# Optimization experiments

Measured on AMD Instinct MI355X. Metric: run time of the kernel, lower is better.

## Reference

```python
import jax, jax.numpy as jnp
import numpy as np
from jax import lax

GAMMA = 1.0
T = 1.0
NEG = -1e30  # acts as -inf for logsumexp padding without producing NaNs in grads


def _dp_forward(D):
    """Soft-max (logsumexp) 2D DP: R[i,j] = D[i,j] + LSE(R[i-1,j-1], R[i-1,j], R[i,j-1]).
    D: [B, N, M] -> R: [B, N, M]. Implemented with a padded virtual row/col where
    R_pad[0,0]=0 and all other boundary cells are NEG (-inf surrogate)."""
    B, N, M = D.shape
    neg = jnp.full((B,), NEG, D.dtype)

    def row_step(prev, d_row):
        # prev: [B, M+1] padded previous row R_pad[i-1, :]; d_row: [B, M]
        diag = prev[:, :-1]  # R_pad[i-1, j]   (diagonal neighbor of cell j)
        up = prev[:, 1:]     # R_pad[i-1, j+1] (vertical neighbor)

        def col_step(left, xs):
            dg, u, d = xs  # each [B]; left = R_pad[i, j] (horizontal neighbor)
            m = jnp.maximum(jnp.maximum(dg, u), left)
            val = d + m + jnp.log(jnp.exp(dg - m) + jnp.exp(u - m) + jnp.exp(left - m))
            return val, val

        _, row = lax.scan(col_step, neg, (diag.T, up.T, d_row.T))  # row: [M, B]
        row = row.T  # [B, M]
        new_prev = jnp.concatenate([neg[:, None], row], axis=1)  # [B, M+1]
        return new_prev, row

    prev0 = jnp.concatenate(
        [jnp.zeros((B, 1), D.dtype), jnp.full((B, M), NEG, D.dtype)], axis=1
    )  # virtual row: R_pad[0,0]=0, rest -inf
    _, R = lax.scan(row_step, prev0, jnp.swapaxes(D, 0, 1))  # R: [N, B, M]
    return jnp.swapaxes(R, 0, 1)  # [B, N, M]


def setup_inputs() -> dict:
    key = jax.random.key(0)
    d = jax.random.normal(key, (64, 512, 512), dtype=jnp.float32)
    return {"d": d}


def reference(d):
    ds = d / GAMMA
    f = _dp_forward(ds)                           # forward-direction DP
    b = _dp_forward(ds[:, ::-1, ::-1])[:, ::-1, ::-1]  # reverse-direction DP, re-flipped
    logit = f + b - ds
    return GAMMA * (logit - logit.max()) / T
```

## Files before the change

### kernel.cpp

```cpp
#include <hip/hip_runtime.h>
#include <stdint.h>

#define NEGV -1e30f
static constexpr int BATCH = 64;
static constexpr int NN = 512;
static constexpr int MM = 512;
static constexpr int NM = NN * MM;
static constexpr size_t TOTAL = (size_t)BATCH * NM;
static constexpr int ROTC = 11;

typedef float f32x4 __attribute__((ext_vector_type(4)));

__device__ __forceinline__ int prow(int b, int k) {
    return (k + ROTC * b) & 511;
}

__device__ __forceinline__ float wave_shr1(float x) {
    int y = __builtin_amdgcn_mov_dpp(__float_as_int(x), 0x138, 0xf, 0xf, true);
    return __int_as_float(y);
}

#define F4C(v, c) ((c) == 0 ? (v).x : (c) == 1 ? (v).y : (c) == 2 ? (v).z : (v).w)

__device__ __forceinline__ int swz(int row, int c) {
    return row * 64 + ((((c >> 2) ^ (row & 15)) << 2) | (c & 3));
}

__device__ inline float blockMax256(float v) {
    __shared__ float sm[256];
    sm[threadIdx.x] = v;
    __syncthreads();
    for (int s = 128; s > 0; s >>= 1) {
        if ((int)threadIdx.x < s)
            sm[threadIdx.x] = fmaxf(sm[threadIdx.x], sm[threadIdx.x + s]);
        __syncthreads();
    }
    return sm[0];
}


__global__ __launch_bounds__(256) void skew_kernel(const float* __restrict__ D,
                                                   float* __restrict__ Sd) {
    __shared__ float lds[64 * 64];
    const int bi = blockIdx.x;
    const int b = bi >> 6;
    const int t = bi & 63;
    const int r0 = (t >> 3) * 64;
    const int c0 = (t & 7) * 64;
    const float* Db = D + (size_t)b * NM;
    float* So = Sd + (size_t)b * NM;
    {
        const int xg = (threadIdx.x & 15) * 4;
        const int y0 = threadIdx.x >> 4;
        for (int sw = 0; sw < 4; ++sw) {
            const int y = y0 + 16 * sw;
            const float4 v = *(const float4*)(Db + (size_t)(r0 + y) * MM + c0 + xg);
            *(float4*)(lds + swz(y, xg)) = v;
        }
    }
    __syncthreads();
    const int rp = (int)threadIdx.x & 63;
    const int s0 = (int)threadIdx.x >> 6;
    for (int it = 0; it < 32; ++it) {
        const int s = s0 + 4 * it;
        if (s >= 127) break;
        const int dcol = s - rp;
        if (dcol >= 0 && dcol < 64) {
            So[(size_t)prow(b, r0 + c0 + s) * MM + r0 + rp] = lds[swz(rp, dcol)];
        }
    }
}

#define LSE3(dg, up, lf, dd, out) do { \
    const float m_ = fmaxf(fmaxf((dg), (up)), (lf)); \
    const float mn_ = fminf(fminf((dg), (up)), (lf)); \
    const float md_ = __builtin_amdgcn_fmed3f((dg), (up), (lf)); \
    const float s_ = 1.f + __expf(mn_ - m_) + __expf(md_ - m_); \
    (out) = (dd) + m_ + __logf(s_); \
} while (0)

#define D0(RV) (DIR ? (RV)[3] : (RV)[0])
#define D1(RV) (DIR ? (RV)[2] : (RV)[1])
#define D2(RV) (DIR ? (RV)[1] : (RV)[2])
#define D3(RV) (DIR ? (RV)[0] : (RV)[3])

template <int DIR, int HALF>
__device__ __forceinline__ void dp_half(const float* __restrict__ Sdp,
                                        const int b, const int lane,
                                        float* __restrict__ ring,
                                        float2* __restrict__ pring,
                                        volatile int* my_prog,
                                        volatile int* other_prog,
                                        volatile int* w_prog) {
    constexpr int R0 = HALF * 256;
    const int t4 = lane * 4;
    const bool l0 = (lane == 0);

    float pA0 = NEGV, pA1 = NEGV, pA2 = NEGV, pA3 = NEGV;
    float pB0 = NEGV, pB1 = NEGV, pB2 = NEGV, pB3 = NEGV;
    f32x4 r0, r1, r2, r3, r4, r5, r6, r7;

#define RLOAD(kk, RV) do { \
        const int lr_ = DIR ? (510 - (kk)) : (kk); \
        const float* rp_ = Sdp + (size_t)prow(b, lr_) * MM; \
        const float* pa_ = DIR ? (rp_ + 508 - R0 - t4) : (rp_ + R0 + t4); \
        asm volatile("global_load_dwordx4 %0, %1, off" : "=v"(RV) : "v"(pa_)); \
    } while (0)

#define GATE() do { \
        asm volatile("s_waitcnt vmcnt(7)" ::: "memory"); \
        __builtin_amdgcn_sched_barrier(0); \
    } while (0)

#define STEP(PH, PA, PB, RV) do { \
        const int k = kb + (PH); \
        GATE(); \
        const float ups_ = wave_shr1(PA##3); \
        const float dgs_ = wave_shr1(PB##3); \
        float up0_, dg0_; \
        if constexpr (HALF == 0) { \
            up0_ = l0 ? NEGV : ups_; \
            dg0_ = l0 ? ((k == 0) ? 0.f : NEGV) : dgs_; \
        } else { \
            up0_ = l0 ? pr##PH.x : ups_; \
            dg0_ = l0 ? pr##PH.y : dgs_; \
        } \
        const float g1_ = PB##0, g2_ = PB##1, g3_ = PB##2; \
        LSE3(dg0_, up0_, PA##0, D0(RV), PB##0); \
        LSE3(g1_, PA##0, PA##1, D1(RV), PB##1); \
        LSE3(g2_, PA##1, PA##2, D2(RV), PB##2); \
        LSE3(g3_, PA##2, PA##3, D3(RV), PB##3); \
        *(float4*)(ring + ((k & 31) << 9) + R0 + t4) = \
            make_float4(PB##0, PB##1, PB##2, PB##3); \
        if constexpr (HALF == 0) { \
            if (lane == 63) pring[k & 31] = make_float2(PB##3, PA##3); \
        } \
        RLOAD(k + 8, RV); \
    } while (0)

    RLOAD(0, r0); RLOAD(1, r1); RLOAD(2, r2); RLOAD(3, r3);
    RLOAD(4, r4); RLOAD(5, r5); RLOAD(6, r6); RLOAD(7, r7);

    for (int kb = 0; kb < NN + MM; kb += 8) {
        if constexpr (HALF == 0) {
            while (*w_prog < kb - 24 || *other_prog < kb - 24)
                __builtin_amdgcn_s_sleep(2);
        } else {
            while (*other_prog < kb + 6 || *w_prog < kb - 24)
                __builtin_amdgcn_s_sleep(2);
        }
        asm volatile("" ::: "memory");
        float2 pr0 = make_float2(NEGV, NEGV), pr1 = pr0, pr2 = pr0, pr3 = pr0,
               pr4 = pr0, pr5 = pr0, pr6 = pr0, pr7 = pr0;
        if constexpr (HALF == 1) {
            pr0 = pring[(kb - 1) & 31]; pr1 = pring[(kb + 0) & 31];
            pr2 = pring[(kb + 1) & 31]; pr3 = pring[(kb + 2) & 31];
            pr4 = pring[(kb + 3) & 31]; pr5 = pring[(kb + 4) & 31];
            pr6 = pring[(kb + 5) & 31]; pr7 = pring[(kb + 6) & 31];
        }
        STEP(0, pA, pB, r0);
        STEP(1, pB, pA, r1);
        STEP(2, pA, pB, r2);
        STEP(3, pB, pA, r3);
        STEP(4, pA, pB, r4);
        STEP(5, pB, pA, r5);
        STEP(6, pA, pB, r6);
        STEP(7, pB, pA, r7);
        asm volatile("s_waitcnt lgkmcnt(0)" ::: "memory");
        if (l0) *my_prog = kb + 7;
    }

#undef STEP
#undef GATE
#undef RLOAD
}

__device__ __forceinline__ void writer_run(float* __restrict__ Sout, const int b,
                                           const int lane,
                                           const float* __restrict__ ring,
                                           volatile int* a_prog,
                                           volatile int* b_prog,
                                           volatile int* w_prog) {
    const int t8 = lane * 8;
    const int lg0 = lane * 8;
    const int lg1 = lane * 8 + 4;

    float4 v0_0, v1_0, v0_1, v1_1, v0_2, v1_2, v0_3, v1_3,
           v0_4, v1_4, v0_5, v1_5, v0_6, v1_6, v0_7, v1_7;

#define WROW(kk, V0, V1) do { \
        const int k_ = (kk); \
        const float* lp_ = ring + ((k_ & 31) << 9); \
        V0 = *(const float4*)(lp_ + lg0); \
        V1 = *(const float4*)(lp_ + lg1); \
        const int kt_ = k_ - t8; \
        float* sp_ = Sout + (size_t)prow(b, k_) * MM + t8; \
        if (kt_ >= 3 && kt_ <= 511) { \
            *(float4*)sp_ = V0; \
        } else if (kt_ >= 0 && kt_ <= 514) { \
            if (kt_ <= 511)             sp_[0] = V0.x; \
            if (kt_ >= 1 && kt_ <= 512) sp_[1] = V0.y; \
            if (kt_ >= 2 && kt_ <= 513) sp_[2] = V0.z; \
            if (kt_ >= 3)               sp_[3] = V0.w; \
        } \
        if (kt_ >= 7 && kt_ <= 515) { \
            *(float4*)(sp_ + 4) = V1; \
        } else if (kt_ >= 4 && kt_ <= 518) { \
            if (kt_ <= 515)             sp_[4] = V1.x; \
            if (kt_ >= 5 && kt_ <= 516) sp_[5] = V1.y; \
            if (kt_ >= 6 && kt_ <= 517) sp_[6] = V1.z; \
            if (kt_ >= 7)               sp_[7] = V1.w; \
        } \
    } while (0)

    for (int k0 = 0; k0 < NN + MM; k0 += 8) {
        while (*a_prog < k0 + 7 || *b_prog < k0 + 7) __builtin_amdgcn_s_sleep(2);
        asm volatile("" ::: "memory");
        WROW(k0 + 0, v0_0, v1_0);
        WROW(k0 + 1, v0_1, v1_1);
        WROW(k0 + 2, v0_2, v1_2);
        WROW(k0 + 3, v0_3, v1_3);
        WROW(k0 + 4, v0_4, v1_4);
        WROW(k0 + 5, v0_5, v1_5);
        WROW(k0 + 6, v0_6, v1_6);
        WROW(k0 + 7, v0_7, v1_7);
        asm volatile("s_waitcnt lgkmcnt(0)" ::: "memory");
        if (lane == 0) *w_prog = k0 + 7;
    }
#undef WROW
}

__global__ __launch_bounds__(192, 1) void dp_skew_kernel(const float* __restrict__ Sd,
                                                         float* __restrict__ Sf,
                                                         float* __restrict__ Sb) {
    __shared__ float ring[32 * 512];
    __shared__ float2 pring[32];
    __shared__ int ctrl[3];
    if (threadIdx.x == 0) { ctrl[0] = -1; ctrl[1] = -1; ctrl[2] = -1; }
    if (threadIdx.x < 32) pring[threadIdx.x] = make_float2(NEGV, NEGV);
    __syncthreads();

    volatile int* a_prog = &ctrl[0];
    volatile int* b_prog = &ctrl[1];
    volatile int* w_prog = &ctrl[2];

    const int blk = blockIdx.x;
    const int b = blk & (BATCH - 1);
    const int dir = blk >> 6;
    const int wid = (int)threadIdx.x >> 6;
    const int lane = (int)threadIdx.x & 63;
    const float* Sdb = Sd + (size_t)b * NM;
    float* Sout = (dir ? Sb : Sf) + (size_t)b * NM;

    if (wid == 0) {
        if (dir) dp_half<1, 0>(Sdb, b, lane, ring, pring, a_prog, b_prog, w_prog);
        else     dp_half<0, 0>(Sdb, b, lane, ring, pring, a_prog, b_prog, w_prog);
    } else if (wid == 1) {
        if (dir) dp_half<1, 1>(Sdb, b, lane, ring, pring, b_prog, a_prog, w_prog);
        else     dp_half<0, 1>(Sdb, b, lane, ring, pring, b_prog, a_prog, w_prog);
    } else {
        writer_run(Sout, b, lane, ring, a_prog, b_prog, w_prog);
    }
}

__global__ __launch_bounds__(256) void logit_skew_kernel(float* __restrict__ Sd,
                                                         const float* __restrict__ Sf,
                                                         const float* __restrict__ Sb,
                                                         float* __restrict__ partial) {
    const size_t n4 = TOTAL / 4;
    float mx = NEGV;
    const size_t stride = (size_t)gridDim.x * blockDim.x;
    for (size_t e = (size_t)blockIdx.x * blockDim.x + threadIdx.x; e < n4; e += stride) {
        const int b = (int)(e >> 16);
        const int rem = (int)(e & 65535);
        const int kp = rem >> 7;
        const int r4 = (rem & 127) << 2;
        const size_t base = (size_t)b * NM;
        const size_t idx = base + (size_t)prow(b, kp) * MM + r4;
        const float4 f = *(const float4*)(Sf + idx);
        const float4 d = *(const float4*)(Sd + idx);
        const int k2 = (510 - kp) & 511;
        const float4 bb = *(const float4*)(Sb + base + (size_t)prow(b, k2) * MM + (508 - r4));
        float4 v;
        v.x = f.x + bb.w - d.x;
        v.y = f.y + bb.z - d.y;
        v.z = f.z + bb.y - d.z;
        v.w = f.w + bb.x - d.w;
        *(float4*)(Sd + idx) = v;
        mx = fmaxf(mx, fmaxf(fmaxf(v.x, v.y), fmaxf(v.z, v.w)));
    }
    float bm = blockMax256(mx);
    if (threadIdx.x == 0) partial[blockIdx.x] = bm;
}

__global__ __launch_bounds__(256) void finalmax_kernel(const float* __restrict__ partial,
                                                       int n,
                                                       float* __restrict__ outmax) {
    float mx = NEGV;
    for (int i = threadIdx.x; i < n; i += 256) mx = fmaxf(mx, partial[i]);
    float bm = blockMax256(mx);
    if (threadIdx.x == 0) *outmax = bm;
}

__global__ __launch_bounds__(256) void unskew_kernel(const float* __restrict__ OS,
                                                     float* __restrict__ out,
                                                     const float* __restrict__ maxp) {
    __shared__ float lds[127 * 64];
    const float mx = *maxp;
    const int bi = blockIdx.x;
    const int b = bi >> 6;
    const int t = bi & 63;
    const int i0 = (t >> 3) * 64;
    const int j0 = (t & 7) * 64;
    const float* Ob = OS + (size_t)b * NM;
    float* ob = out + (size_t)b * NM;
    const int base = i0 + j0;
    {
        const int xg = ((int)threadIdx.x & 15) * 4;
        const int s0 = (int)threadIdx.x >> 4;
        for (int sw = 0; sw < 8; ++sw) {
            const int s = s0 + 16 * sw;
            if (s < 127) {
                const float4 v = *(const float4*)(Ob + (size_t)prow(b, base + s) * MM + i0 + xg);
                *(float4*)(lds + swz(s, xg)) = v;
            }
        }
    }
    __syncthreads();
    const int x4 = ((int)threadIdx.x & 15) * 4;
    const int y0 = (int)threadIdx.x >> 4;
    for (int sw = 0; sw < 4; ++sw) {
        const int y = y0 + 16 * sw;
        float4 v;
        v.x = lds[swz(x4 + 0 + y, y)] - mx;
        v.y = lds[swz(x4 + 1 + y, y)] - mx;
        v.z = lds[swz(x4 + 2 + y, y)] - mx;
        v.w = lds[swz(x4 + 3 + y, y)] - mx;
        *(float4*)(ob + (size_t)(i0 + y) * MM + j0 + x4) = v;
    }
}

template <int DIR>
__device__ __forceinline__ void dp_run_legacy(const float* __restrict__ Db,
                                              float* __restrict__ Rp, int lane) {
    const int i0 = lane * 8;
    const bool l0 = (lane == 0);
    const float dgb0 = l0 ? 0.f : NEGV;

#define PTRS(r) \
    const float* ldp_##r = DIR ? (Db + (size_t)(NM - 1) - (size_t)(i0 + r) * MM) \
                               : (Db + (size_t)(i0 + r) * MM); \
    float* stp_##r = DIR ? (Rp + (size_t)(NM - 1) - (size_t)(i0 + r) * MM) \
                         : (Rp + (size_t)(i0 + r) * MM);
    PTRS(0) PTRS(1) PTRS(2) PTRS(3) PTRS(4) PTRS(5) PTRS(6) PTRS(7)

#define LOADG(r, dst, jgexpr) do { \
        int jc_ = (jgexpr); \
        jc_ = jc_ < 0 ? 0 : jc_; jc_ = jc_ > (MM - 4) ? (MM - 4) : jc_; \
        if (DIR) { const float4 t_ = *(const float4*)(ldp_##r - jc_ - 3); \
                   dst = make_float4(t_.w, t_.z, t_.y, t_.x); } \
        else     { dst = *(const float4*)(ldp_##r + jc_); } \
    } while (0)

#define INIT(r) \
    float p1_##r = NEGV, p2_##r = NEGV, p3_##r = NEGV, np_##r = NEGV; \
    float4 dc_##r, dn_##r; \
    LOADG(r, dn_##r, 0); dc_##r = dn_##r;
    INIT(0) INIT(1) INIT(2) INIT(3) INIT(4) INIT(5) INIT(6) INIT(7)

#define SWAPLOAD(r) do { dc_##r = dn_##r; LOADG(r, dn_##r, jj - (r) + 4); } while (0)

#define CELL(r, KK, DGIN, UPIN, DGB) do { \
        const int j_ = jj - (r); \
        const bool jz_ = (j_ == 0); \
        const float dg_ = jz_ ? (DGB) : (DGIN); \
        const float up_ = (UPIN); \
        const float lf_ = jz_ ? NEGV : p1_##r; \
        const float m_  = fmaxf(fmaxf(dg_, up_), lf_); \
        const float mn_ = fminf(fminf(dg_, up_), lf_); \
        const float md_ = __builtin_amdgcn_fmed3f(dg_, up_, lf_); \
        const float s_  = 1.f + __expf(mn_ - m_) + __expf(md_ - m_); \
        np_##r = F4C(dc_##r, ((KK) - (r)) & 3) + m_ + __logf(s_); \
    } while (0)

#define STORE(r) do { \
        const int j_ = jj - (r); \
        if (j_ >= 3 && j_ < MM) { \
            if (DIR) *(float4*)(stp_##r - j_) = \
                make_float4(np_##r, p1_##r, p2_##r, p3_##r); \
            else     *(float4*)(stp_##r + j_ - 3) = \
                make_float4(p3_##r, p2_##r, p1_##r, np_##r); \
        } \
    } while (0)

#define SHIFT(r) do { p3_##r = p2_##r; p2_##r = p1_##r; p1_##r = np_##r; } while (0)

#define LSTEP(KK, LA, LB, SA, SB) do { \
        const int jj = kbj + (KK); \
        SWAPLOAD(LA); SWAPLOAD(LB); \
        const float ups_ = wave_shr1(p1_7); \
        const float dgs_ = wave_shr1(p2_7); \
        const float up0r = l0 ? NEGV : ups_; \
        const float dg0r = l0 ? NEGV : dgs_; \
        CELL(0, KK, dg0r, up0r, dgb0); \
        CELL(1, KK, p2_0, p1_0, NEGV); \
        CELL(2, KK, p2_1, p1_1, NEGV); \
        CELL(3, KK, p2_2, p1_2, NEGV); \
        CELL(4, KK, p2_3, p1_3, NEGV); \
        CELL(5, KK, p2_4, p1_4, NEGV); \
        CELL(6, KK, p2_5, p1_5, NEGV); \
        CELL(7, KK, p2_6, p1_6, NEGV); \
        STORE(SA); STORE(SB); \
        SHIFT(0); SHIFT(1); SHIFT(2); SHIFT(3); \
        SHIFT(4); SHIFT(5); SHIFT(6); SHIFT(7); \
    } while (0)

    for (int kb = 0; kb < NN + MM; kb += 4) {
        const int kbj = kb - i0;
        LSTEP(0, 0, 4, 1, 5);
        LSTEP(1, 1, 5, 2, 6);
        LSTEP(2, 2, 6, 3, 7);
        LSTEP(3, 3, 7, 0, 4);
    }

#undef PTRS
#undef LOADG
#undef INIT
#undef SWAPLOAD
#undef CELL
#undef STORE
#undef SHIFT
#undef LSTEP
}

__global__ __launch_bounds__(64, 1) void dp_kernel_legacy(const float* __restrict__ D,
                                                          float* __restrict__ Rf,
                                                          float* __restrict__ Rb) {
    const int blk = blockIdx.x;
    const int b = blk & (BATCH - 1);
    const int dir = blk >> 6;
    const float* __restrict__ Db = D + (size_t)b * NM;
    const int lane = (int)threadIdx.x;
    if (dir) dp_run_legacy<1>(Db, Rb + (size_t)b * NM, lane);
    else     dp_run_legacy<0>(Db, Rf + (size_t)b * NM, lane);
}

__global__ __launch_bounds__(256) void logit_kernel(const float4* __restrict__ D,
                                                    const float4* __restrict__ Rb,
                                                    float4* __restrict__ out,
                                                    float* __restrict__ partial) {
    const size_t n4 = TOTAL / 4;
    float mx = NEGV;
    const size_t stride = (size_t)gridDim.x * blockDim.x;
    for (size_t idx = (size_t)blockIdx.x * blockDim.x + threadIdx.x; idx < n4;
         idx += stride) {
        float4 f = out[idx], bb = Rb[idx], d = D[idx];
        float4 v = make_float4(f.x + bb.x - d.x, f.y + bb.y - d.y,
                               f.z + bb.z - d.z, f.w + bb.w - d.w);
        out[idx] = v;
        mx = fmaxf(mx, fmaxf(fmaxf(v.x, v.y), fmaxf(v.z, v.w)));
    }
    float bm = blockMax256(mx);
    if (threadIdx.x == 0) partial[blockIdx.x] = bm;
}

__global__ __launch_bounds__(256) void sub_kernel(float4* __restrict__ out,
                                                  const float* __restrict__ maxp) {
    const float mx = *maxp;
    const size_t n4 = TOTAL / 4;
    const size_t stride = (size_t)gridDim.x * blockDim.x;
    for (size_t idx = (size_t)blockIdx.x * blockDim.x + threadIdx.x; idx < n4;
         idx += stride) {
        float4 v = out[idx];
        v.x -= mx; v.y -= mx; v.z -= mx; v.w -= mx;
        out[idx] = v;
    }
}

extern "C" void kernel_launch(void* const* d_in, const int* in_sizes, int n_in,
                              void* d_out, int out_size, void* d_ws, size_t ws_size,
                              hipStream_t stream) {
    const float* D = (const float*)d_in[0];
    float* out = (float*)d_out;

    const size_t needed = (2 * TOTAL + 4096) * sizeof(float);
    if (ws_size >= needed) {
        float* Sd = (float*)d_ws;
        float* Sb = Sd + TOTAL;
        float* partial = Sd + 2 * TOTAL;
        float* maxp = partial + 2048;

        skew_kernel<<<4096, 256, 0, stream>>>(D, Sd);
        dp_skew_kernel<<<128, 192, 0, stream>>>(Sd, out, Sb);
        logit_skew_kernel<<<2048, 256, 0, stream>>>(Sd, out, Sb, partial);
        finalmax_kernel<<<1, 256, 0, stream>>>(partial, 2048, maxp);
        unskew_kernel<<<4096, 256, 0, stream>>>(Sd, out, maxp);
    } else {
        float* Rb = (float*)d_ws;
        float* partial = Rb + TOTAL;
        float* maxp = partial + 2048;

        dp_kernel_legacy<<<128, 64, 0, stream>>>(D, out, Rb);
        logit_kernel<<<2048, 256, 0, stream>>>((const float4*)D, (const float4*)Rb,
                                               (float4*)out, partial);
        finalmax_kernel<<<1, 256, 0, stream>>>(partial, 2048, maxp);
        sub_kernel<<<2048, 256, 0, stream>>>((float4*)out, maxp);
    }
}
```

Measured before the change: 516.6 us.

## Split DP wavefront across four waves of 128 columns each

The anti-diagonal DP per batch/direction now runs on four compute waves instead of two, with each lane handling 2 cells instead of 4. Boundary values pass between neighbouring waves through per-pair LDS rings, and progress flags chain the waves together. The aim is to shorten the serial per-step LSE chain per lane on a latency-bound kernel. The cost is more inter-wave synchronisation, a pipeline fill delay that grows with the chain depth, and narrower dwordx2 loads.

```diff
diff --git a/kernel.cpp b/kernel.cpp
--- a/kernel.cpp
+++ b/kernel.cpp
@@ -10,6 +10,7 @@
 static constexpr int ROTC = 11;
 
 typedef float f32x4 __attribute__((ext_vector_type(4)));
+typedef float f32x2 __attribute__((ext_vector_type(2)));
 
 __device__ __forceinline__ int prow(int b, int k) {
     return (k + ROTC * b) & 511;
@@ -79,32 +80,32 @@
     (out) = (dd) + m_ + __logf(s_); \
 } while (0)
 
-#define D0(RV) (DIR ? (RV)[3] : (RV)[0])
-#define D1(RV) (DIR ? (RV)[2] : (RV)[1])
-#define D2(RV) (DIR ? (RV)[1] : (RV)[2])
-#define D3(RV) (DIR ? (RV)[0] : (RV)[3])
-
-template <int DIR, int HALF>
-__device__ __forceinline__ void dp_half(const float* __restrict__ Sdp,
-                                        const int b, const int lane,
-                                        float* __restrict__ ring,
-                                        float2* __restrict__ pring,
-                                        volatile int* my_prog,
-                                        volatile int* other_prog,
-                                        volatile int* w_prog) {
-    constexpr int R0 = HALF * 256;
-    const int t4 = lane * 4;
+#define D0(RV) (DIR ? (RV)[1] : (RV)[0])
+#define D1(RV) (DIR ? (RV)[0] : (RV)[1])
+
+template <int DIR, int Q>
+__device__ __forceinline__ void dp_quarter(const float* __restrict__ Sdp,
+                                           const int b, const int lane,
+                                           float* __restrict__ ring,
+                                           float2* __restrict__ pr_prev,
+                                           float2* __restrict__ pr_next,
+                                           volatile int* my_prog,
+                                           volatile int* prev_prog,
+                                           volatile int* next_prog,
+                                           volatile int* w_prog) {
+    constexpr int R0 = Q * 128;
+    const int t2 = lane * 2;
     const bool l0 = (lane == 0);
 
-    float pA0 = NEGV, pA1 = NEGV, pA2 = NEGV, pA3 = NEGV;
-    float pB0 = NEGV, pB1 = NEGV, pB2 = NEGV, pB3 = NEGV;
-    f32x4 r0, r1, r2, r3, r4, r5, r6, r7;
+    float pA0 = NEGV, pA1 = NEGV;
+    float pB0 = NEGV, pB1 = NEGV;
+    f32x2 r0, r1, r2, r3, r4, r5, r6, r7;
 
 #define RLOAD(kk, RV) do { \
         const int lr_ = DIR ? (510 - (kk)) : (kk); \
         const float* rp_ = Sdp + (size_t)prow(b, lr_) * MM; \
-        const float* pa_ = DIR ? (rp_ + 508 - R0 - t4) : (rp_ + R0 + t4); \
-        asm volatile("global_load_dwordx4 %0, %1, off" : "=v"(RV) : "v"(pa_)); \
+        const float* pa_ = DIR ? (rp_ + 510 - R0 - t2) : (rp_ + R0 + t2); \
+        asm volatile("global_load_dwordx2 %0, %1, off" : "=v"(RV) : "v"(pa_)); \
     } while (0)
 
 #define GATE() do { \
@@ -115,25 +116,22 @@
 #define STEP(PH, PA, PB, RV) do { \
         const int k = kb + (PH); \
         GATE(); \
-        const float ups_ = wave_shr1(PA##3); \
-        const float dgs_ = wave_shr1(PB##3); \
+        const float ups_ = wave_shr1(PA##1); \
+        const float dgs_ = wave_shr1(PB##1); \
         float up0_, dg0_; \
-        if constexpr (HALF == 0) { \
+        if constexpr (Q == 0) { \
             up0_ = l0 ? NEGV : ups_; \
             dg0_ = l0 ? ((k == 0) ? 0.f : NEGV) : dgs_; \
         } else { \
             up0_ = l0 ? pr##PH.x : ups_; \
             dg0_ = l0 ? pr##PH.y : dgs_; \
         } \
-        const float g1_ = PB##0, g2_ = PB##1, g3_ = PB##2; \
+        const float g1_ = PB##0; \
         LSE3(dg0_, up0_, PA##0, D0(RV), PB##0); \
         LSE3(g1_, PA##0, PA##1, D1(RV), PB##1); \
-        LSE3(g2_, PA##1, PA##2, D2(RV), PB##2); \
-        LSE3(g3_, PA##2, PA##3, D3(RV), PB##3); \
-        *(float4*)(ring + ((k & 31) << 9) + R0 + t4) = \
-            make_float4(PB##0, PB##1, PB##2, PB##3); \
-        if constexpr (HALF == 0) { \
-            if (lane == 63) pring[k & 31] = make_float2(PB##3, PA##3); \
+        *(float2*)(ring + ((k & 31) << 9) + R0 + t2) = make_float2(PB##0, PB##1); \
+        if constexpr (Q < 3) { \
+            if (lane == 63) pr_next[k & 31] = make_float2(PB##1, PA##1); \
         } \
         RLOAD(k + 8, RV); \
     } while (0)
@@ -142,21 +140,21 @@
     RLOAD(4, r4); RLOAD(5, r5); RLOAD(6, r6); RLOAD(7, r7);
 
     for (int kb = 0; kb < NN + MM; kb += 8) {
-        if constexpr (HALF == 0) {
-            while (*w_prog < kb - 24 || *other_prog < kb - 24)
-                __builtin_amdgcn_s_sleep(2);
-        } else {
-            while (*other_prog < kb + 6 || *w_prog < kb - 24)
-                __builtin_amdgcn_s_sleep(2);
+        for (;;) {
+            bool ok = (*w_prog >= kb - 24);
+            if constexpr (Q > 0) ok = ok && (*prev_prog >= kb + 6);
+            if constexpr (Q < 3) ok = ok && (*next_prog >= kb - 24);
+            if (ok) break;
+            __builtin_amdgcn_s_sleep(2);
         }
         asm volatile("" ::: "memory");
         float2 pr0 = make_float2(NEGV, NEGV), pr1 = pr0, pr2 = pr0, pr3 = pr0,
                pr4 = pr0, pr5 = pr0, pr6 = pr0, pr7 = pr0;
-        if constexpr (HALF == 1) {
-            pr0 = pring[(kb - 1) & 31]; pr1 = pring[(kb + 0) & 31];
-            pr2 = pring[(kb + 1) & 31]; pr3 = pring[(kb + 2) & 31];
-            pr4 = pring[(kb + 3) & 31]; pr5 = pring[(kb + 4) & 31];
-            pr6 = pring[(kb + 5) & 31]; pr7 = pring[(kb + 6) & 31];
+        if constexpr (Q > 0) {
+            pr0 = pr_prev[(kb - 1) & 31]; pr1 = pr_prev[(kb + 0) & 31];
+            pr2 = pr_prev[(kb + 1) & 31]; pr3 = pr_prev[(kb + 2) & 31];
+            pr4 = pr_prev[(kb + 3) & 31]; pr5 = pr_prev[(kb + 4) & 31];
+            pr6 = pr_prev[(kb + 5) & 31]; pr7 = pr_prev[(kb + 6) & 31];
         }
         STEP(0, pA, pB, r0);
         STEP(1, pB, pA, r1);
@@ -178,8 +176,7 @@
 __device__ __forceinline__ void writer_run(float* __restrict__ Sout, const int b,
                                            const int lane,
                                            const float* __restrict__ ring,
-                                           volatile int* a_prog,
-                                           volatile int* b_prog,
+                                           volatile int* p3_prog,
                                            volatile int* w_prog) {
     const int t8 = lane * 8;
     const int lg0 = lane * 8;
@@ -214,7 +211,7 @@
     } while (0)
 
     for (int k0 = 0; k0 < NN + MM; k0 += 8) {
-        while (*a_prog < k0 + 7 || *b_prog < k0 + 7) __builtin_amdgcn_s_sleep(2);
+        while (*p3_prog < k0 + 7) __builtin_amdgcn_s_sleep(2);
         asm volatile("" ::: "memory");
         WROW(k0 + 0, v0_0, v1_0);
         WROW(k0 + 1, v0_1, v1_1);
@@ -230,19 +227,19 @@
 #undef WROW
 }
 
-__global__ __launch_bounds__(192, 1) void dp_skew_kernel(const float* __restrict__ Sd,
+__global__ __launch_bounds__(320, 1) void dp_skew_kernel(const float* __restrict__ Sd,
                                                          float* __restrict__ Sf,
                                                          float* __restrict__ Sb) {
     __shared__ float ring[32 * 512];
-    __shared__ float2 pring[32];
-    __shared__ int ctrl[3];
-    if (threadIdx.x == 0) { ctrl[0] = -1; ctrl[1] = -1; ctrl[2] = -1; }
-    if (threadIdx.x < 32) pring[threadIdx.x] = make_float2(NEGV, NEGV);
+    __shared__ float2 pring[3][32];
+    __shared__ int ctrl[5];
+    if (threadIdx.x < 5) ctrl[threadIdx.x] = -1;
+    if (threadIdx.x < 96) pring[threadIdx.x / 32][threadIdx.x & 31] =
+        make_float2(NEGV, NEGV);
     __syncthreads();
 
-    volatile int* a_prog = &ctrl[0];
-    volatile int* b_prog = &ctrl[1];
-    volatile int* w_prog = &ctrl[2];
+    volatile int* prog = (volatile int*)ctrl;
+    volatile int* w_prog = &((volatile int*)ctrl)[4];
 
     const int blk = blockIdx.x;
     const int b = blk & (BATCH - 1);
@@ -253,13 +250,27 @@
     float* Sout = (dir ? Sb : Sf) + (size_t)b * NM;
 
     if (wid == 0) {
-        if (dir) dp_half<1, 0>(Sdb, b, lane, ring, pring, a_prog, b_prog, w_prog);
-        else     dp_half<0, 0>(Sdb, b, lane, ring, pring, a_prog, b_prog, w_prog);
+        if (dir) dp_quarter<1, 0>(Sdb, b, lane, ring, nullptr, pring[0],
+                                  &prog[0], nullptr, &prog[1], w_prog);
+        else     dp_quarter<0, 0>(Sdb, b, lane, ring, nullptr, pring[0],
+                                  &prog[0], nullptr, &prog[1], w_prog);
     } else if (wid == 1) {
-        if (dir) dp_half<1, 1>(Sdb, b, lane, ring, pring, b_prog, a_prog, w_prog);
-        else     dp_half<0, 1>(Sdb, b, lane, ring, pring, b_prog, a_prog, w_prog);
+        if (dir) dp_quarter<1, 1>(Sdb, b, lane, ring, pring[0], pring[1],
+                                  &prog[1], &prog[0], &prog[2], w_prog);
+        else     dp_quarter<0, 1>(Sdb, b, lane, ring, pring[0], pring[1],
+                                  &prog[1], &prog[0], &prog[2], w_prog);
+    } else if (wid == 2) {
+        if (dir) dp_quarter<1, 2>(Sdb, b, lane, ring, pring[1], pring[2],
+                                  &prog[2], &prog[1], &prog[3], w_prog);
+        else     dp_quarter<0, 2>(Sdb, b, lane, ring, pring[1], pring[2],
+                                  &prog[2], &prog[1], &prog[3], w_prog);
+    } else if (wid == 3) {
+        if (dir) dp_quarter<1, 3>(Sdb, b, lane, ring, pring[2], nullptr,
+                                  &prog[3], &prog[2], nullptr, w_prog);
+        else     dp_quarter<0, 3>(Sdb, b, lane, ring, pring[2], nullptr,
+                                  &prog[3], &prog[2], nullptr, w_prog);
     } else {
-        writer_run(Sout, b, lane, ring, a_prog, b_prog, w_prog);
+        writer_run(Sout, b, lane, ring, &prog[3], w_prog);
     }
 }
 
@@ -491,7 +502,7 @@
         float* maxp = partial + 2048;
 
         skew_kernel<<<4096, 256, 0, stream>>>(D, Sd);
-        dp_skew_kernel<<<128, 192, 0, stream>>>(Sd, out, Sb);
+        dp_skew_kernel<<<128, 320, 0, stream>>>(Sd, out, Sb);
         logit_skew_kernel<<<2048, 256, 0, stream>>>(Sd, out, Sb, partial);
         finalmax_kernel<<<1, 256, 0, stream>>>(partial, 2048, maxp);
         unskew_kernel<<<4096, 256, 0, stream>>>(Sd, out, maxp);
```

New measurement: 548.0 us. +6.1%, slower.
